# Kernel tuning notes

Hardware: AMD Instinct MI355X
Metric: run time of the kernel (lower is better)

Reference implementation:

```python
import jax, jax.numpy as jnp
import numpy as np

N_NODES = 100000
N_EDGES = 1600000
D = 64
N_GRAPHS = 64


def setup_inputs() -> dict:
    key = jax.random.key(0)
    ks = jax.random.split(key, 8)
    x = jax.random.normal(ks[0], (N_NODES, D), dtype=jnp.float32)
    edge_index = jax.random.randint(ks[1], (2, N_EDGES), 0, N_NODES)
    batch = jnp.sort(jax.random.randint(ks[2], (N_NODES,), 0, N_GRAPHS))
    edge_weight = jax.random.uniform(ks[3], (N_EDGES,), dtype=jnp.float32)
    s = 1.0 / np.sqrt(D)
    W1 = jax.random.normal(ks[4], (D, D), dtype=jnp.float32) * s
    b1 = jnp.zeros((D,), dtype=jnp.float32)
    W2 = jax.random.normal(ks[5], (D, D), dtype=jnp.float32) * s
    b2 = jnp.zeros((D,), dtype=jnp.float32)
    return {"x": x, "edge_index": edge_index, "batch": batch,
            "edge_weight": edge_weight, "W1": W1, "b1": b1, "W2": W2, "b2": b2}


def reference(x, edge_index, batch, edge_weight, W1, b1, W2, b2):
    # --- GCN normalization with self-loops (PyG gcn_norm, fill_value=1) ---
    loop = jnp.arange(N_NODES)
    src = jnp.concatenate([edge_index[0], loop])
    dst = jnp.concatenate([edge_index[1], loop])
    ew = jnp.concatenate([edge_weight, jnp.ones((N_NODES,), x.dtype)])
    deg = jax.ops.segment_sum(ew, dst, num_segments=N_NODES)
    dinv = jnp.where(deg > 0, jax.lax.rsqrt(deg), 0.0)
    norm = dinv[src] * ew * dinv[dst]  # [E+N]

    def gcn_relu(h, W, b):
        h = h @ W                                   # [N, D]
        msg = h[src] * norm[:, None]                # gather + weight messages
        agg = jax.ops.segment_sum(msg, dst, num_segments=N_NODES)
        return jax.nn.relu(agg + b)

    h = gcn_relu(x, W1, b1)
    h = gcn_relu(h, W2, b2)

    # --- global mean pool over graphs ---
    sums = jax.ops.segment_sum(h, batch, num_segments=N_GRAPHS)
    counts = jax.ops.segment_sum(jnp.ones((N_NODES, 1), h.dtype), batch,
                                 num_segments=N_GRAPHS)
    return sums / jnp.maximum(counts, 1.0)
```

## Files before the change

kernel.cpp:

```cpp
#include <hip/hip_runtime.h>

#define N_NODES 100000
#define N_EDGES 1600000
#define D 64
#define N_GRAPHS 64
#define NBLK ((N_NODES + 255) / 256)
#define WTS 68

__global__ void k_init(float* __restrict__ deg, int* __restrict__ cnt,
                       float* __restrict__ out) {
    int i = blockIdx.x * blockDim.x + threadIdx.x;
    if (i < N_NODES) { deg[i] = 1.0f; cnt[i] = 0; }
    if (i < N_GRAPHS * D) out[i] = 0.0f;
}

__global__ void k_count_deg(const int* __restrict__ dst, const float* __restrict__ ew,
                            float* __restrict__ deg, int* __restrict__ cnt) {
    int e = blockIdx.x * blockDim.x + threadIdx.x;
    if (e < N_EDGES) {
        int d = dst[e];
        atomicAdd(&deg[d], ew[e]);
        atomicAdd(&cnt[d], 1);
    }
}

__global__ void k_dinv(float* __restrict__ deg) {
    int i = blockIdx.x * blockDim.x + threadIdx.x;
    if (i < N_NODES) {
        float d = deg[i];
        deg[i] = d > 0.f ? rsqrtf(d) : 0.f;
    }
}

__global__ void k_scan1(const int* __restrict__ cnt, int* __restrict__ partial,
                        int* __restrict__ bsums) {
    int t = threadIdx.x, b = blockIdx.x, i = b * 256 + t;
    int v = (i < N_NODES) ? cnt[i] : 0;
    int incl = v;
    int lane = t & 63;
#pragma unroll
    for (int off = 1; off < 64; off <<= 1) {
        int u = __shfl_up(incl, off);
        if (lane >= off) incl += u;
    }
    __shared__ int wsum[4];
    int w = t >> 6;
    if (lane == 63) wsum[w] = incl;
    __syncthreads();
    int add = 0;
    for (int k = 0; k < w; ++k) add += wsum[k];
    incl += add;
    if (i < N_NODES) partial[i] = incl;
    if (t == 255) bsums[b] = incl;
}

__global__ void k_scan2(int* __restrict__ bsums) {
    __shared__ int s[512];
    int t = threadIdx.x;
    s[t] = (t < NBLK) ? bsums[t] : 0;
    __syncthreads();
    for (int off = 1; off < 512; off <<= 1) {
        int u = (t >= off) ? s[t - off] : 0;
        __syncthreads();
        s[t] += u;
        __syncthreads();
    }
    if (t < NBLK) bsums[t] = (t == 0) ? 0 : s[t - 1];
}

__global__ void k_scan3(const int* __restrict__ partial, const int* __restrict__ cnt,
                        const int* __restrict__ bsums, int* __restrict__ rowptr,
                        int* __restrict__ cursor) {
    int i = blockIdx.x * 256 + threadIdx.x;
    if (i < N_NODES) {
        int excl = partial[i] - cnt[i] + bsums[blockIdx.x];
        rowptr[i] = excl;
        cursor[i] = excl;
    }
}

__global__ void k_scatter(const int* __restrict__ src, const int* __restrict__ dst,
                          const float* __restrict__ ew, const float* __restrict__ dinv,
                          int* __restrict__ cursor, float2* __restrict__ csr) {
    int e = blockIdx.x * blockDim.x + threadIdx.x;
    if (e < N_EDGES) {
        int s = src[e];
        int d = dst[e];
        float nrm = dinv[s] * ew[e] * dinv[d];
        int pos = atomicAdd(&cursor[d], 1);
        csr[pos] = make_float2(__int_as_float(s), nrm);
    }
}

template <int LAYER>
__global__ __launch_bounds__(256) void k_layer(
        const float* __restrict__ in, const float* __restrict__ W,
        const float* __restrict__ bias, const float* __restrict__ dinv,
        const int* __restrict__ rowptr, const int* __restrict__ cnt,
        const float2* __restrict__ csr, const int* __restrict__ batch,
        float* __restrict__ outp) {
    __shared__ float WTs[D * WTS];
    __shared__ float aw[4][WTS];
    __shared__ float bs[D];

    {
        int t = threadIdx.x;
#pragma unroll
        for (int i = 0; i < 16; ++i) {
            int idx = t + i * 256;
            int k = idx >> 6, c = idx & 63;
            WTs[c * WTS + k] = W[idx];
        }
        if (t < D) bs[t] = bias[t];
    }
    __syncthreads();

    const int lane = threadIdx.x & 63;
    const int wid  = threadIdx.x >> 6;
    float* awm = aw[wid];
    const float bl = bs[lane];

    int gw = (blockIdx.x * blockDim.x + threadIdx.x) >> 6;
    const int tw = (gridDim.x * blockDim.x) >> 6;

    for (int row = gw; row < N_NODES; row += tw) {
        const int st = __builtin_amdgcn_readfirstlane(rowptr[row]);
        const int dg = __builtin_amdgcn_readfirstlane(cnt[row]);
        float di = dinv[row];
        float acc = in[row * D + lane] * (di * di);

        int j = 0;
        for (; j + 8 <= dg; j += 8) {
            float2 e0 = csr[st + j + 0];
            float2 e1 = csr[st + j + 1];
            float2 e2 = csr[st + j + 2];
            float2 e3 = csr[st + j + 3];
            float2 e4 = csr[st + j + 4];
            float2 e5 = csr[st + j + 5];
            float2 e6 = csr[st + j + 6];
            float2 e7 = csr[st + j + 7];
            int s0 = __builtin_amdgcn_readfirstlane(__float_as_int(e0.x));
            int s1 = __builtin_amdgcn_readfirstlane(__float_as_int(e1.x));
            int s2 = __builtin_amdgcn_readfirstlane(__float_as_int(e2.x));
            int s3 = __builtin_amdgcn_readfirstlane(__float_as_int(e3.x));
            int s4 = __builtin_amdgcn_readfirstlane(__float_as_int(e4.x));
            int s5 = __builtin_amdgcn_readfirstlane(__float_as_int(e5.x));
            int s6 = __builtin_amdgcn_readfirstlane(__float_as_int(e6.x));
            int s7 = __builtin_amdgcn_readfirstlane(__float_as_int(e7.x));
            float v0 = in[s0 * D + lane];
            float v1 = in[s1 * D + lane];
            float v2 = in[s2 * D + lane];
            float v3 = in[s3 * D + lane];
            float v4 = in[s4 * D + lane];
            float v5 = in[s5 * D + lane];
            float v6 = in[s6 * D + lane];
            float v7 = in[s7 * D + lane];
            acc = fmaf(v0, e0.y, acc);
            acc = fmaf(v1, e1.y, acc);
            acc = fmaf(v2, e2.y, acc);
            acc = fmaf(v3, e3.y, acc);
            acc = fmaf(v4, e4.y, acc);
            acc = fmaf(v5, e5.y, acc);
            acc = fmaf(v6, e6.y, acc);
            acc = fmaf(v7, e7.y, acc);
        }
        for (; j < dg; ++j) {
            float2 e = csr[st + j];
            int s0 = __builtin_amdgcn_readfirstlane(__float_as_int(e.x));
            acc = fmaf(in[s0 * D + lane], e.y, acc);
        }

        awm[lane] = acc;
        float r0 = 0.f, r1 = 0.f, r2 = 0.f, r3 = 0.f;
#pragma unroll
        for (int t = 0; t < 16; ++t) {
            float4 a = *(const float4*)&awm[t * 4];
            float4 w = *(const float4*)&WTs[lane * WTS + t * 4];
            r0 = fmaf(a.x, w.x, r0);
            r1 = fmaf(a.y, w.y, r1);
            r2 = fmaf(a.z, w.z, r2);
            r3 = fmaf(a.w, w.w, r3);
        }
        float r = fmaxf((r0 + r1) + (r2 + r3) + bl, 0.f);

        if (LAYER == 1) {
            outp[row * D + lane] = r;
        } else {
            atomicAdd(&outp[batch[row] * D + lane], r);
        }
    }
}

__global__ void k_finalize(float* __restrict__ out, const int* __restrict__ batch) {
    int g = blockIdx.x;
    int lane = threadIdx.x;
    int lo = 0, hi = N_NODES;
    while (lo < hi) { int m = (lo + hi) >> 1; if (batch[m] < g) lo = m + 1; else hi = m; }
    int start = lo;
    hi = N_NODES;
    while (lo < hi) { int m = (lo + hi) >> 1; if (batch[m] < g + 1) lo = m + 1; else hi = m; }
    float c = (float)(lo - start);
    out[g * D + lane] /= fmaxf(c, 1.0f);
}

extern "C" void kernel_launch(void* const* d_in, const int* in_sizes, int n_in,
                              void* d_out, int out_size, void* d_ws, size_t ws_size,
                              hipStream_t stream) {
    const float* x     = (const float*)d_in[0];
    const int*   ei    = (const int*)d_in[1];
    const int*   src   = ei;
    const int*   dst   = ei + N_EDGES;
    const int*   batch = (const int*)d_in[2];
    const float* ew    = (const float*)d_in[3];
    const float* W1    = (const float*)d_in[4];
    const float* b1    = (const float*)d_in[5];
    const float* W2    = (const float*)d_in[6];
    const float* b2    = (const float*)d_in[7];
    float* out = (float*)d_out;

    char* ws = (char*)d_ws;
    float*  bufA   = (float*)(ws);
    float2* csr    = (float2*)(ws + 25600000);
    float*  deg    = (float*)(ws + 38400000);
    int*    cnt    = (int*)(ws + 38800000);
    int*    rowptr = (int*)(ws + 39200000);
    int*    cursor = (int*)(ws + 39600000);
    int*    bsums  = (int*)(ws + 40000000);

    k_init<<<NBLK, 256, 0, stream>>>(deg, cnt, out);
    k_count_deg<<<(N_EDGES + 255) / 256, 256, 0, stream>>>(dst, ew, deg, cnt);
    k_dinv<<<NBLK, 256, 0, stream>>>(deg);
    k_scan1<<<NBLK, 256, 0, stream>>>(cnt, rowptr, bsums);
    k_scan2<<<1, 512, 0, stream>>>(bsums);
    k_scan3<<<NBLK, 256, 0, stream>>>(rowptr, cnt, bsums, rowptr, cursor);
    k_scatter<<<(N_EDGES + 255) / 256, 256, 0, stream>>>(src, dst, ew, deg, cursor, csr);

    k_layer<1><<<2048, 256, 0, stream>>>(x, W1, b1, deg, rowptr, cnt, csr, batch, bufA);
    k_layer<2><<<2048, 256, 0, stream>>>(bufA, W2, b2, deg, rowptr, cnt, csr, batch, out);
    k_finalize<<<N_GRAPHS, D, 0, stream>>>(out, batch);
}
```

Measured before the change: 523.0 us.

## Prefetch next row's CSR edges into double-buffered LDS and fuse dinv into scan

Each wavefront now loads the next row's edge list (up to 128 entries) with one coalesced load into registers while it processes the current row, then stores it into a double-buffered LDS slot. The inner gather loop reads edge entries from LDS, with masked tails, instead of issuing scalar-dependent global loads. The dinv computation is merged into the first scan kernel to drop one launch. This adds LDS use and masked wasted gathers in tail passes, and it relies on wave-local LDS ordering without explicit barriers.

```diff
diff --git a/kernel.cpp b/kernel.cpp
--- a/kernel.cpp
+++ b/kernel.cpp
@@ -6,6 +6,7 @@
 #define N_GRAPHS 64
 #define NBLK ((N_NODES + 255) / 256)
 #define WTS 68
+#define NBUF 128
 
 __global__ void k_init(float* __restrict__ deg, int* __restrict__ cnt,
                        float* __restrict__ out) {
@@ -24,17 +25,13 @@
     }
 }
 
-__global__ void k_dinv(float* __restrict__ deg) {
-    int i = blockIdx.x * blockDim.x + threadIdx.x;
+__global__ void k_scan1(const int* __restrict__ cnt, int* __restrict__ partial,
+                        int* __restrict__ bsums, float* __restrict__ deg) {
+    int t = threadIdx.x, b = blockIdx.x, i = b * 256 + t;
     if (i < N_NODES) {
         float d = deg[i];
         deg[i] = d > 0.f ? rsqrtf(d) : 0.f;
     }
-}
-
-__global__ void k_scan1(const int* __restrict__ cnt, int* __restrict__ partial,
-                        int* __restrict__ bsums) {
-    int t = threadIdx.x, b = blockIdx.x, i = b * 256 + t;
     int v = (i < N_NODES) ? cnt[i] : 0;
     int incl = v;
     int lane = t & 63;
@@ -99,9 +96,10 @@
         const int* __restrict__ rowptr, const int* __restrict__ cnt,
         const float2* __restrict__ csr, const int* __restrict__ batch,
         float* __restrict__ outp) {
-    __shared__ float WTs[D * WTS];
-    __shared__ float aw[4][WTS];
-    __shared__ float bs[D];
+    __shared__ float  WTs[D * WTS];
+    __shared__ float  aw[4][D];
+    __shared__ float2 ebuf[4][2][NBUF];
+    __shared__ float  bs[D];
 
     {
         int t = threadIdx.x;
@@ -117,28 +115,62 @@
 
     const int lane = threadIdx.x & 63;
     const int wid  = threadIdx.x >> 6;
-    float* awm = aw[wid];
+    float*  awm = aw[wid];
+    float2 (*eb)[NBUF] = ebuf[wid];
     const float bl = bs[lane];
 
     int gw = (blockIdx.x * blockDim.x + threadIdx.x) >> 6;
     const int tw = (gridDim.x * blockDim.x) >> 6;
 
-    for (int row = gw; row < N_NODES; row += tw) {
-        const int st = __builtin_amdgcn_readfirstlane(rowptr[row]);
-        const int dg = __builtin_amdgcn_readfirstlane(cnt[row]);
+    int row = gw;
+    int st = 0, dg = 0, cur = 0;
+
+    if (row < N_NODES) {
+        st = __builtin_amdgcn_readfirstlane(rowptr[row]);
+        dg = __builtin_amdgcn_readfirstlane(cnt[row]);
+        int ne = dg < NBUF ? dg : NBUF;
+        float2 mA, mB;
+        if (lane < ne)      mA = csr[st + lane];
+        if (64 + lane < ne) mB = csr[st + 64 + lane];
+        if (lane < ne)      eb[0][lane] = mA;
+        if (64 + lane < ne) eb[0][64 + lane] = mB;
+    }
+
+    for (; row < N_NODES; row += tw) {
+        const int nrow = row + tw;
+        int stn = 0, dgn = 0, nen = 0;
+        float2 mA = make_float2(0.f, 0.f), mB = make_float2(0.f, 0.f);
+        if (nrow < N_NODES) {
+            stn = __builtin_amdgcn_readfirstlane(rowptr[nrow]);
+            dgn = __builtin_amdgcn_readfirstlane(cnt[nrow]);
+            nen = dgn < NBUF ? dgn : NBUF;
+            if (lane < nen)      mA = csr[stn + lane];
+            if (64 + lane < nen) mB = csr[stn + 64 + lane];
+        }
+
         float di = dinv[row];
         float acc = in[row * D + lane] * (di * di);
-
-        int j = 0;
-        for (; j + 8 <= dg; j += 8) {
-            float2 e0 = csr[st + j + 0];
-            float2 e1 = csr[st + j + 1];
-            float2 e2 = csr[st + j + 2];
-            float2 e3 = csr[st + j + 3];
-            float2 e4 = csr[st + j + 4];
-            float2 e5 = csr[st + j + 5];
-            float2 e6 = csr[st + j + 6];
-            float2 e7 = csr[st + j + 7];
+        const float2* ebf = eb[cur];
+        const int ne = dg < NBUF ? dg : NBUF;
+        const int passes = (ne + 7) >> 3;
+        for (int p = 0; p < passes; ++p) {
+            const int j = p * 8;
+            float2 e0 = ebf[(j + 0 < ne) ? j + 0 : 0];
+            float2 e1 = ebf[(j + 1 < ne) ? j + 1 : 0];
+            float2 e2 = ebf[(j + 2 < ne) ? j + 2 : 0];
+            float2 e3 = ebf[(j + 3 < ne) ? j + 3 : 0];
+            float2 e4 = ebf[(j + 4 < ne) ? j + 4 : 0];
+            float2 e5 = ebf[(j + 5 < ne) ? j + 5 : 0];
+            float2 e6 = ebf[(j + 6 < ne) ? j + 6 : 0];
+            float2 e7 = ebf[(j + 7 < ne) ? j + 7 : 0];
+            float w0 = (j + 0 < ne) ? e0.y : 0.f;
+            float w1 = (j + 1 < ne) ? e1.y : 0.f;
+            float w2 = (j + 2 < ne) ? e2.y : 0.f;
+            float w3 = (j + 3 < ne) ? e3.y : 0.f;
+            float w4 = (j + 4 < ne) ? e4.y : 0.f;
+            float w5 = (j + 5 < ne) ? e5.y : 0.f;
+            float w6 = (j + 6 < ne) ? e6.y : 0.f;
+            float w7 = (j + 7 < ne) ? e7.y : 0.f;
             int s0 = __builtin_amdgcn_readfirstlane(__float_as_int(e0.x));
             int s1 = __builtin_amdgcn_readfirstlane(__float_as_int(e1.x));
             int s2 = __builtin_amdgcn_readfirstlane(__float_as_int(e2.x));
@@ -155,19 +187,25 @@
             float v5 = in[s5 * D + lane];
             float v6 = in[s6 * D + lane];
             float v7 = in[s7 * D + lane];
-            acc = fmaf(v0, e0.y, acc);
-            acc = fmaf(v1, e1.y, acc);
-            acc = fmaf(v2, e2.y, acc);
-            acc = fmaf(v3, e3.y, acc);
-            acc = fmaf(v4, e4.y, acc);
-            acc = fmaf(v5, e5.y, acc);
-            acc = fmaf(v6, e6.y, acc);
-            acc = fmaf(v7, e7.y, acc);
-        }
-        for (; j < dg; ++j) {
+            acc = fmaf(v0, w0, acc);
+            acc = fmaf(v1, w1, acc);
+            acc = fmaf(v2, w2, acc);
+            acc = fmaf(v3, w3, acc);
+            acc = fmaf(v4, w4, acc);
+            acc = fmaf(v5, w5, acc);
+            acc = fmaf(v6, w6, acc);
+            acc = fmaf(v7, w7, acc);
+        }
+        for (int j = NBUF; j < dg; ++j) {
             float2 e = csr[st + j];
-            int s0 = __builtin_amdgcn_readfirstlane(__float_as_int(e.x));
-            acc = fmaf(in[s0 * D + lane], e.y, acc);
+            int s = __builtin_amdgcn_readfirstlane(__float_as_int(e.x));
+            acc = fmaf(in[s * D + lane], e.y, acc);
+        }
+
+        {
+            float2* ebn = eb[cur ^ 1];
+            if (lane < nen)      ebn[lane] = mA;
+            if (64 + lane < nen) ebn[64 + lane] = mB;
         }
 
         awm[lane] = acc;
@@ -188,6 +226,8 @@
         } else {
             atomicAdd(&outp[batch[row] * D + lane], r);
         }
+
+        st = stn; dg = dgn; cur ^= 1;
     }
 }
 
@@ -229,8 +269,7 @@
 
     k_init<<<NBLK, 256, 0, stream>>>(deg, cnt, out);
     k_count_deg<<<(N_EDGES + 255) / 256, 256, 0, stream>>>(dst, ew, deg, cnt);
-    k_dinv<<<NBLK, 256, 0, stream>>>(deg);
-    k_scan1<<<NBLK, 256, 0, stream>>>(cnt, rowptr, bsums);
+    k_scan1<<<NBLK, 256, 0, stream>>>(cnt, rowptr, bsums, deg);
     k_scan2<<<1, 512, 0, stream>>>(bsums);
     k_scan3<<<NBLK, 256, 0, stream>>>(rowptr, cnt, bsums, rowptr, cursor);
     k_scatter<<<(N_EDGES + 255) / 256, 256, 0, stream>>>(src, dst, ew, deg, cursor, csr);
```

Result: faster. 498.5 us (-4.7%).

## Gather four neighbor rows per wavefront with float4 loads, fold dinv into scan

Applied to the files above, without the earlier changes.

The aggregation loop now splits each 64-lane wavefront into four 16-lane slots. Each slot gathers a different neighbor row with float4 loads, and neighbor indices and weights are broadcast via shuffles from one coalesced CSR load per 16 edges. The partial sums are combined by xor-shuffle reduction before the dense transform. This is meant to raise memory-level parallelism and cut the number of serialized scalar index reads per edge. It also drops the init and dinv kernels by using memsets and computing rsqrt(deg+1) inside the first scan kernel, at the cost of padded, masked work for low-degree rows.

```diff
diff --git a/kernel.cpp b/kernel.cpp
--- a/kernel.cpp
+++ b/kernel.cpp
@@ -6,13 +6,6 @@
 #define N_GRAPHS 64
 #define NBLK ((N_NODES + 255) / 256)
 #define WTS 68
-
-__global__ void k_init(float* __restrict__ deg, int* __restrict__ cnt,
-                       float* __restrict__ out) {
-    int i = blockIdx.x * blockDim.x + threadIdx.x;
-    if (i < N_NODES) { deg[i] = 1.0f; cnt[i] = 0; }
-    if (i < N_GRAPHS * D) out[i] = 0.0f;
-}
 
 __global__ void k_count_deg(const int* __restrict__ dst, const float* __restrict__ ew,
                             float* __restrict__ deg, int* __restrict__ cnt) {
@@ -24,17 +17,13 @@
     }
 }
 
-__global__ void k_dinv(float* __restrict__ deg) {
-    int i = blockIdx.x * blockDim.x + threadIdx.x;
+__global__ void k_scan1(const int* __restrict__ cnt, int* __restrict__ partial,
+                        int* __restrict__ bsums, float* __restrict__ deg) {
+    int t = threadIdx.x, b = blockIdx.x, i = b * 256 + t;
     if (i < N_NODES) {
         float d = deg[i];
-        deg[i] = d > 0.f ? rsqrtf(d) : 0.f;
-    }
-}
-
-__global__ void k_scan1(const int* __restrict__ cnt, int* __restrict__ partial,
-                        int* __restrict__ bsums) {
-    int t = threadIdx.x, b = blockIdx.x, i = b * 256 + t;
+        deg[i] = rsqrtf(d + 1.0f);
+    }
     int v = (i < N_NODES) ? cnt[i] : 0;
     int incl = v;
     int lane = t & 63;
@@ -100,7 +89,7 @@
         const float2* __restrict__ csr, const int* __restrict__ batch,
         float* __restrict__ outp) {
     __shared__ float WTs[D * WTS];
-    __shared__ float aw[4][WTS];
+    __shared__ float aw[4][D];
     __shared__ float bs[D];
 
     {
@@ -117,8 +106,11 @@
 
     const int lane = threadIdx.x & 63;
     const int wid  = threadIdx.x >> 6;
+    const int slot = lane >> 4;
+    const int q    = lane & 15;
     float* awm = aw[wid];
     const float bl = bs[lane];
+    const float4* in4 = (const float4*)in;
 
     int gw = (blockIdx.x * blockDim.x + threadIdx.x) >> 6;
     const int tw = (gridDim.x * blockDim.x) >> 6;
@@ -126,51 +118,58 @@
     for (int row = gw; row < N_NODES; row += tw) {
         const int st = __builtin_amdgcn_readfirstlane(rowptr[row]);
         const int dg = __builtin_amdgcn_readfirstlane(cnt[row]);
-        float di = dinv[row];
-        float acc = in[row * D + lane] * (di * di);
-
-        int j = 0;
-        for (; j + 8 <= dg; j += 8) {
-            float2 e0 = csr[st + j + 0];
-            float2 e1 = csr[st + j + 1];
-            float2 e2 = csr[st + j + 2];
-            float2 e3 = csr[st + j + 3];
-            float2 e4 = csr[st + j + 4];
-            float2 e5 = csr[st + j + 5];
-            float2 e6 = csr[st + j + 6];
-            float2 e7 = csr[st + j + 7];
-            int s0 = __builtin_amdgcn_readfirstlane(__float_as_int(e0.x));
-            int s1 = __builtin_amdgcn_readfirstlane(__float_as_int(e1.x));
-            int s2 = __builtin_amdgcn_readfirstlane(__float_as_int(e2.x));
-            int s3 = __builtin_amdgcn_readfirstlane(__float_as_int(e3.x));
-            int s4 = __builtin_amdgcn_readfirstlane(__float_as_int(e4.x));
-            int s5 = __builtin_amdgcn_readfirstlane(__float_as_int(e5.x));
-            int s6 = __builtin_amdgcn_readfirstlane(__float_as_int(e6.x));
-            int s7 = __builtin_amdgcn_readfirstlane(__float_as_int(e7.x));
-            float v0 = in[s0 * D + lane];
-            float v1 = in[s1 * D + lane];
-            float v2 = in[s2 * D + lane];
-            float v3 = in[s3 * D + lane];
-            float v4 = in[s4 * D + lane];
-            float v5 = in[s5 * D + lane];
-            float v6 = in[s6 * D + lane];
-            float v7 = in[s7 * D + lane];
-            acc = fmaf(v0, e0.y, acc);
-            acc = fmaf(v1, e1.y, acc);
-            acc = fmaf(v2, e2.y, acc);
-            acc = fmaf(v3, e3.y, acc);
-            acc = fmaf(v4, e4.y, acc);
-            acc = fmaf(v5, e5.y, acc);
-            acc = fmaf(v6, e6.y, acc);
-            acc = fmaf(v7, e7.y, acc);
-        }
-        for (; j < dg; ++j) {
-            float2 e = csr[st + j];
-            int s0 = __builtin_amdgcn_readfirstlane(__float_as_int(e.x));
-            acc = fmaf(in[s0 * D + lane], e.y, acc);
-        }
-
-        awm[lane] = acc;
+        const int dgm1 = dg - 1;
+
+        float4 acc = make_float4(0.f, 0.f, 0.f, 0.f);
+        {
+            float di = dinv[row];
+            if (slot == 0) {
+                float4 s4 = in4[row * 16 + q];
+                float d2 = di * di;
+                acc.x = s4.x * d2; acc.y = s4.y * d2;
+                acc.z = s4.z * d2; acc.w = s4.w * d2;
+            }
+        }
+
+        for (int j = 0; j < dg; j += 16) {
+            int ie = j + q;
+            float2 c = csr[st + (ie < dgm1 ? ie : dgm1)];
+            float sx0 = __shfl(c.x, 4 * 0 + slot);
+            float wv0 = __shfl(c.y, 4 * 0 + slot);
+            float sx1 = __shfl(c.x, 4 * 1 + slot);
+            float wv1 = __shfl(c.y, 4 * 1 + slot);
+            float sx2 = __shfl(c.x, 4 * 2 + slot);
+            float wv2 = __shfl(c.y, 4 * 2 + slot);
+            float sx3 = __shfl(c.x, 4 * 3 + slot);
+            float wv3 = __shfl(c.y, 4 * 3 + slot);
+            wv0 = (j + 0 + slot  < dg) ? wv0 : 0.f;
+            wv1 = (j + 4 + slot  < dg) ? wv1 : 0.f;
+            wv2 = (j + 8 + slot  < dg) ? wv2 : 0.f;
+            wv3 = (j + 12 + slot < dg) ? wv3 : 0.f;
+            int i0 = __float_as_int(sx0);
+            int i1 = __float_as_int(sx1);
+            int i2 = __float_as_int(sx2);
+            int i3 = __float_as_int(sx3);
+            float4 v0 = in4[i0 * 16 + q];
+            float4 v1 = in4[i1 * 16 + q];
+            float4 v2 = in4[i2 * 16 + q];
+            float4 v3 = in4[i3 * 16 + q];
+            acc.x = fmaf(v0.x, wv0, acc.x); acc.y = fmaf(v0.y, wv0, acc.y);
+            acc.z = fmaf(v0.z, wv0, acc.z); acc.w = fmaf(v0.w, wv0, acc.w);
+            acc.x = fmaf(v1.x, wv1, acc.x); acc.y = fmaf(v1.y, wv1, acc.y);
+            acc.z = fmaf(v1.z, wv1, acc.z); acc.w = fmaf(v1.w, wv1, acc.w);
+            acc.x = fmaf(v2.x, wv2, acc.x); acc.y = fmaf(v2.y, wv2, acc.y);
+            acc.z = fmaf(v2.z, wv2, acc.z); acc.w = fmaf(v2.w, wv2, acc.w);
+            acc.x = fmaf(v3.x, wv3, acc.x); acc.y = fmaf(v3.y, wv3, acc.y);
+            acc.z = fmaf(v3.z, wv3, acc.z); acc.w = fmaf(v3.w, wv3, acc.w);
+        }
+
+        acc.x += __shfl_xor(acc.x, 16); acc.y += __shfl_xor(acc.y, 16);
+        acc.z += __shfl_xor(acc.z, 16); acc.w += __shfl_xor(acc.w, 16);
+        acc.x += __shfl_xor(acc.x, 32); acc.y += __shfl_xor(acc.y, 32);
+        acc.z += __shfl_xor(acc.z, 32); acc.w += __shfl_xor(acc.w, 32);
+        if (slot == 0) *(float4*)&awm[q * 4] = acc;
+
         float r0 = 0.f, r1 = 0.f, r2 = 0.f, r3 = 0.f;
 #pragma unroll
         for (int t = 0; t < 16; ++t) {
@@ -227,10 +226,12 @@
     int*    cursor = (int*)(ws + 39600000);
     int*    bsums  = (int*)(ws + 40000000);
 
-    k_init<<<NBLK, 256, 0, stream>>>(deg, cnt, out);
+    hipMemsetAsync(deg, 0, N_NODES * sizeof(float), stream);
+    hipMemsetAsync(cnt, 0, N_NODES * sizeof(int), stream);
+    hipMemsetAsync(out, 0, N_GRAPHS * D * sizeof(float), stream);
+
     k_count_deg<<<(N_EDGES + 255) / 256, 256, 0, stream>>>(dst, ew, deg, cnt);
-    k_dinv<<<NBLK, 256, 0, stream>>>(deg);
-    k_scan1<<<NBLK, 256, 0, stream>>>(cnt, rowptr, bsums);
+    k_scan1<<<NBLK, 256, 0, stream>>>(cnt, rowptr, bsums, deg);
     k_scan2<<<1, 512, 0, stream>>>(bsums);
     k_scan3<<<NBLK, 256, 0, stream>>>(rowptr, cnt, bsums, rowptr, cursor);
     k_scatter<<<(N_EDGES + 255) / 256, 256, 0, stream>>>(src, dst, ew, deg, cursor, csr);
```

Measured after the change: 508.1 us. 2.9% less time.
